# Performance work log

Measured on AMD Instinct MI355X. Metric: run time of the kernel, lower is better.

## Reference

```python
import jax, jax.numpy as jnp
import numpy as np

HEAD_SIZE = 64

def setup_inputs() -> dict:
    key = jax.random.key(0)
    k1, k2, k3, k4 = jax.random.split(key, 4)
    B, T, C, H = 8, 2048, 1024, HEAD_SIZE
    x = jax.random.normal(k1, (B, T, C), dtype=jnp.float32)
    attention_mask = jnp.ones((B, T), dtype=jnp.int32)
    # nn.Linear(C, H, bias=False): store as [C, H] so y = x @ W
    s = 1.0 / np.sqrt(C)
    Wk = jax.random.normal(k2, (C, H), dtype=jnp.float32) * s
    Wq = jax.random.normal(k3, (C, H), dtype=jnp.float32) * s
    Wv = jax.random.normal(k4, (C, H), dtype=jnp.float32) * s
    return {"x": x, "attention_mask": attention_mask, "Wk": Wk, "Wq": Wq, "Wv": Wv}

def reference(x, attention_mask, Wk, Wq, Wv):
    # x: [B, T, C]; projections -> [B, T, H]
    k = jnp.einsum('btc,ch->bth', x, Wk)
    q = jnp.einsum('btc,ch->bth', x, Wq)
    v = jnp.einsum('btc,ch->bth', x, Wv)
    scale = k.shape[-1] ** -0.5
    wei = jnp.einsum('bqh,bkh->bqk', q, k) * scale  # [B, T, T]
    mask = attention_mask[:, None, :]               # [B, 1, T] key-padding mask
    wei = jnp.where(mask == 0, -jnp.inf, wei)
    wei_soft = jax.nn.softmax(wei, axis=-1)
    # dropout p=0.0 (eval mode): identity
    out = jnp.einsum('bqk,bkh->bqh', wei_soft, v)   # [B, T, H]
    return out
```

## Files before the change

### kernel.cpp

```cpp
#include <hip/hip_runtime.h>
#include <hip/hip_bf16.h>

typedef __bf16 bf16;
typedef __bf16 bf16x4 __attribute__((ext_vector_type(4)));
typedef __bf16 bf16x8 __attribute__((ext_vector_type(8)));
typedef float f32x4 __attribute__((ext_vector_type(4)));

#define NB 8
#define NT 2048
#define NC 1024
#define NH 64

__device__ inline f32x4 zero4() {
    f32x4 z; z[0] = 0.f; z[1] = 0.f; z[2] = 0.f; z[3] = 0.f; return z;
}

__global__ __launch_bounds__(256) void pack_w(const float* __restrict__ Wq,
                                              const float* __restrict__ Wk,
                                              const float* __restrict__ Wv,
                                              bf16* __restrict__ Wt2) {
    const int g = blockIdx.x * 256 + threadIdx.x;
    const int l = g & 63;
    const int kc = (g >> 6) & 1;
    const int kt = (g >> 7) & 15;
    const int nf = g >> 11;
    const int n = nf * 16 + (l & 15);
    const int k0 = kt * 64 + kc * 32 + (l >> 4) * 8;
    const float* W = (n < 64) ? Wq : (n < 128) ? Wk : Wv;
    const int h = n & 63;
    bf16x8 o;
#pragma unroll
    for (int e = 0; e < 8; ++e) o[e] = (bf16)W[(k0 + e) * NH + h];
    *reinterpret_cast<bf16x8*>(Wt2 + (size_t)g * 8) = o;
}

__global__ __launch_bounds__(256, 2) void qkv_gemm(const float* __restrict__ x,
                                                   const bf16* __restrict__ Wt2,
                                                   bf16* __restrict__ qp,
                                                   bf16* __restrict__ kp2,
                                                   bf16* __restrict__ vt2) {
    __shared__ bf16 xs[2][64][72];
    const int tid = threadIdx.x;
    const int wave = tid >> 6, lane = tid & 63;
    const int l16 = lane & 15, lhi = lane >> 4;
    const int qh = wave & 1;
    const int ch = wave >> 1;
    const int row0 = blockIdx.x * 64;
    const bf16* wb = Wt2 + (size_t)ch * 98304 + lane * 8;

    f32x4 acc[2][6];
#pragma unroll
    for (int mr = 0; mr < 2; ++mr)
#pragma unroll
        for (int nf = 0; nf < 6; ++nf) acc[mr][nf] = zero4();

    const int sr = tid >> 4;
    const int sc = (tid & 15) * 4;

    float4 xv[3][4];
    bf16x8 bfr[2][12];

#define LOAD_X(SLOT, KT)  do { \
    _Pragma("unroll") for (int _i = 0; _i < 4; ++_i) \
        xv[SLOT][_i] = *reinterpret_cast<const float4*>( \
            &x[(size_t)(row0 + sr + _i * 16) * NC + (KT) * 64 + sc]); \
} while (0)

#define LOAD_B(SLOT, KT)  do { \
    _Pragma("unroll") for (int _nf = 0; _nf < 6; ++_nf) \
        _Pragma("unroll") for (int _kc = 0; _kc < 2; ++_kc) \
            bfr[SLOT][_nf * 2 + _kc] = *reinterpret_cast<const bf16x8*>( \
                wb + _nf * 16384 + (KT) * 1024 + _kc * 512); \
} while (0)

#define WRITE_XS(BUF, SLOT)  do { \
    _Pragma("unroll") for (int _i = 0; _i < 4; ++_i) { \
        bf16x4 _w; \
        _w[0] = (bf16)xv[SLOT][_i].x; _w[1] = (bf16)xv[SLOT][_i].y; \
        _w[2] = (bf16)xv[SLOT][_i].z; _w[3] = (bf16)xv[SLOT][_i].w; \
        *reinterpret_cast<bf16x4*>(&xs[BUF][sr + _i * 16][sc]) = _w; \
    } \
} while (0)

    LOAD_X(0, 0);
    LOAD_X(1, 1);
    LOAD_X(2, 2);
    LOAD_B(0, 0);
    WRITE_XS(0, 0);
    __syncthreads();

#pragma unroll
    for (int kt = 0; kt < 16; ++kt) {
        const int cur = kt & 1, nxt = cur ^ 1;
        if (kt < 13) LOAD_X(kt % 3, kt + 3);
        bf16x8 a[2][2];
#pragma unroll
        for (int mr = 0; mr < 2; ++mr)
#pragma unroll
            for (int kc = 0; kc < 2; ++kc)
                a[mr][kc] = *reinterpret_cast<const bf16x8*>(
                    &xs[cur][qh * 32 + mr * 16 + l16][kc * 32 + lhi * 8]);
        if (kt < 15) WRITE_XS(nxt, (kt + 1) % 3);
        if (kt < 15) LOAD_B(nxt, kt + 1);
        __syncthreads();
        __builtin_amdgcn_s_setprio(1);
#pragma unroll
        for (int nf = 0; nf < 6; ++nf)
#pragma unroll
            for (int kc = 0; kc < 2; ++kc)
#pragma unroll
                for (int mr = 0; mr < 2; ++mr)
                    acc[mr][nf] = __builtin_amdgcn_mfma_f32_16x16x32_bf16(
                        a[mr][kc], bfr[cur][nf * 2 + kc], acc[mr][nf], 0, 0, 0);
        __builtin_amdgcn_s_setprio(0);
    }
#undef LOAD_X
#undef LOAD_B
#undef WRITE_XS

#pragma unroll
    for (int mr = 0; mr < 2; ++mr)
#pragma unroll
    for (int nf = 0; nf < 6; ++nf) {
        const int col = ch * 96 + nf * 16 + l16;
#pragma unroll
        for (int r = 0; r < 4; ++r) {
            const int row = row0 + qh * 32 + mr * 16 + lhi * 4 + r;
            const bf16 val = (bf16)acc[mr][nf][r];
            const int bb = row >> 11, kv = row & (NT - 1);
            const int t = kv >> 6;
            if (col < 64) {
                qp[(size_t)row * NH + col] = val;
            } else if (col < 128) {
                const int h = col - 64;
                const int kvb = (kv >> 4) & 3;
                const int lK = ((h & 31) >> 3) * 16 + (kv & 15);
                kp2[((((size_t)(bb * 32 + t) * 4 + kvb) * 2 + (h >> 5)) * 64 + lK) * 8 + (h & 7)] = val;
            } else {
                const int h = col - 128;
                const int kcV = (kv >> 5) & 1;
                const int lV = ((kv & 31) >> 3) * 16 + (h & 15);
                vt2[((((size_t)(bb * 32 + t) * 2 + kcV) * 4 + (h >> 4)) * 64 + lV) * 8 + (kv & 7)] = val;
            }
        }
    }
}

__global__ __launch_bounds__(256, 2) void attn(const bf16* __restrict__ qp,
                                               const bf16* __restrict__ kp2,
                                               const bf16* __restrict__ vt2,
                                               const int* __restrict__ mask,
                                               float* __restrict__ out) {
    __shared__ __align__(16) char smem[4 * 2 * 16 * 68 * 4];
    bf16 (*p_lds)[64][20] = reinterpret_cast<bf16 (*)[64][20]>(smem);
    float (*sm_o)[2][16][68] = reinterpret_cast<float (*)[2][16][68]>(smem);
    __shared__ float sm_m[4][2][16], sm_l[4][2][16];

    const int tid = threadIdx.x;
    const int sp = tid >> 6, lane = tid & 63;
    const int l16 = lane & 15, lhi = lane >> 4;
    const int b = blockIdx.y;
    const int tb = sp * 8;
    bf16* const pw = &p_lds[sp][0][0];

    bf16x8 aq[2][2];
#pragma unroll
    for (int t = 0; t < 2; ++t)
#pragma unroll
        for (int hc = 0; hc < 2; ++hc)
            aq[t][hc] = *reinterpret_cast<const bf16x8*>(
                &qp[((size_t)b * NT + blockIdx.x * 32 + t * 16 + l16) * NH + hc * 32 + lhi * 8]);

    const bf16* kw = kp2 + (size_t)b * 131072 + (size_t)tb * 4096 + lane * 8;
    const bf16* vw = vt2 + (size_t)b * 131072 + (size_t)tb * 4096 + lane * 8;
    const int*  mw = mask + b * NT + tb * 64 + lhi * 4;

    float m[2] = {-1e30f, -1e30f}, l[2] = {0.f, 0.f};
    f32x4 o[2][4];
#pragma unroll
    for (int t = 0; t < 2; ++t)
#pragma unroll
        for (int hb = 0; hb < 4; ++hb) o[t][hb] = zero4();

#pragma unroll
    for (int it = 0; it < 8; ++it) {
        const int fo = it * 4096;
        bf16x8 kf[8];
#pragma unroll
        for (int i = 0; i < 8; ++i)
            kf[i] = *reinterpret_cast<const bf16x8*>(kw + fo + i * 512);
        int4 mv[4];
#pragma unroll
        for (int kvb = 0; kvb < 4; ++kvb)
            mv[kvb] = *reinterpret_cast<const int4*>(mw + it * 64 + kvb * 16);
        f32x4 s[2][4];
        __builtin_amdgcn_s_setprio(1);
#pragma unroll
        for (int t = 0; t < 2; ++t)
#pragma unroll
            for (int kvb = 0; kvb < 4; ++kvb) {
                s[t][kvb] = zero4();
                s[t][kvb] = __builtin_amdgcn_mfma_f32_16x16x32_bf16(kf[kvb * 2], aq[t][0], s[t][kvb], 0, 0, 0);
                s[t][kvb] = __builtin_amdgcn_mfma_f32_16x16x32_bf16(kf[kvb * 2 + 1], aq[t][1], s[t][kvb], 0, 0, 0);
            }
        __builtin_amdgcn_s_setprio(0);
        bf16x8 vf[8];
#pragma unroll
        for (int i = 0; i < 8; ++i)
            vf[i] = *reinterpret_cast<const bf16x8*>(vw + fo + i * 512);
#pragma unroll
        for (int t = 0; t < 2; ++t)
#pragma unroll
            for (int kvb = 0; kvb < 4; ++kvb) {
                s[t][kvb][0] = mv[kvb].x ? s[t][kvb][0] * 0.125f : -1e30f;
                s[t][kvb][1] = mv[kvb].y ? s[t][kvb][1] * 0.125f : -1e30f;
                s[t][kvb][2] = mv[kvb].z ? s[t][kvb][2] * 0.125f : -1e30f;
                s[t][kvb][3] = mv[kvb].w ? s[t][kvb][3] * 0.125f : -1e30f;
            }
#pragma unroll
        for (int t = 0; t < 2; ++t) {
            float tm = s[t][0][0];
#pragma unroll
            for (int kvb = 0; kvb < 4; ++kvb)
#pragma unroll
                for (int r = 0; r < 4; ++r) tm = fmaxf(tm, s[t][kvb][r]);
            tm = fmaxf(tm, __shfl_xor(tm, 16));
            tm = fmaxf(tm, __shfl_xor(tm, 32));
            const float mn = fmaxf(m[t], tm);
            const float alpha = __expf(m[t] - mn);
            m[t] = mn;
            float ps = 0.f;
#pragma unroll
            for (int kvb = 0; kvb < 4; ++kvb)
#pragma unroll
                for (int r = 0; r < 4; ++r) {
                    const float p = __expf(s[t][kvb][r] - m[t]);
                    s[t][kvb][r] = p;
                    ps += p;
                }
            ps += __shfl_xor(ps, 16);
            ps += __shfl_xor(ps, 32);
            l[t] = l[t] * alpha + ps;
#pragma unroll
            for (int kvb = 0; kvb < 4; ++kvb) {
                bf16x4 w;
                w[0] = (bf16)s[t][kvb][0]; w[1] = (bf16)s[t][kvb][1];
                w[2] = (bf16)s[t][kvb][2]; w[3] = (bf16)s[t][kvb][3];
                const int row = l16 + 16 * ((kvb * 2 + (lhi >> 1)) & 3);
                *reinterpret_cast<bf16x4*>(pw + row * 20 + (kvb >> 1) * 8 + (lhi & 1) * 4) = w;
            }
            float ar[4];
#pragma unroll
            for (int r = 0; r < 4; ++r) ar[r] = __shfl(alpha, lhi * 4 + r);
#pragma unroll
            for (int hb = 0; hb < 4; ++hb)
#pragma unroll
                for (int r = 0; r < 4; ++r) o[t][hb][r] *= ar[r];
            __builtin_amdgcn_s_setprio(1);
#pragma unroll
            for (int kc = 0; kc < 2; ++kc) {
                const bf16* pr = pw + lane * 20 + kc * 8;
                const bf16x4 lo = *reinterpret_cast<const bf16x4*>(pr);
                const bf16x4 hi = *reinterpret_cast<const bf16x4*>(pr + 4);
                const bf16x8 pa = __builtin_shufflevector(lo, hi, 0, 1, 2, 3, 4, 5, 6, 7);
#pragma unroll
                for (int hb = 0; hb < 4; ++hb)
                    o[t][hb] = __builtin_amdgcn_mfma_f32_16x16x32_bf16(pa, vf[kc * 4 + hb], o[t][hb], 0, 0, 0);
            }
            __builtin_amdgcn_s_setprio(0);
        }
    }

    __syncthreads();
#pragma unroll
    for (int t = 0; t < 2; ++t) {
#pragma unroll
        for (int hb = 0; hb < 4; ++hb)
#pragma unroll
            for (int r = 0; r < 4; ++r)
                sm_o[sp][t][lhi * 4 + r][hb * 16 + l16] = o[t][hb][r];
        if (lhi == 0) {
            sm_m[sp][t][l16] = m[t];
            sm_l[sp][t][l16] = l[t];
        }
    }
    __syncthreads();

#pragma unroll
    for (int e = 0; e < 8; ++e) {
        const int idx = e * 256 + tid;
        const int row = idx >> 6;
        const int col = idx & 63;
        const int t2 = row >> 4, r16 = row & 15;
        float M = sm_m[0][t2][r16];
#pragma unroll
        for (int s2 = 1; s2 < 4; ++s2) M = fmaxf(M, sm_m[s2][t2][r16]);
        float L = 0.f, accv = 0.f;
#pragma unroll
        for (int s2 = 0; s2 < 4; ++s2) {
            const float w = __expf(sm_m[s2][t2][r16] - M);
            L += w * sm_l[s2][t2][r16];
            accv += w * sm_o[s2][t2][r16][col];
        }
        out[((size_t)b * NT + blockIdx.x * 32 + row) * NH + col] = accv / L;
    }
}

extern "C" void kernel_launch(void* const* d_in, const int* in_sizes, int n_in,
                              void* d_out, int out_size, void* d_ws, size_t ws_size,
                              hipStream_t stream) {
    const float* x    = (const float*)d_in[0];
    const int*   mask = (const int*)d_in[1];
    const float* Wk   = (const float*)d_in[2];
    const float* Wq   = (const float*)d_in[3];
    const float* Wv   = (const float*)d_in[4];
    float* out = (float*)d_out;

    char* ws = (char*)d_ws;
    bf16* Wt2 = (bf16*)(ws);
    bf16* qp  = (bf16*)(ws + (512 << 10));
    bf16* kp2 = (bf16*)(ws + (512 << 10) + (2 << 20));
    bf16* vt2 = (bf16*)(ws + (512 << 10) + (4 << 20));

    pack_w<<<dim3(96), dim3(256), 0, stream>>>(Wq, Wk, Wv, Wt2);
    qkv_gemm<<<dim3(256), dim3(256), 0, stream>>>(x, Wt2, qp, kp2, vt2);
    attn<<<dim3(64, 8), dim3(256), 0, stream>>>(qp, kp2, vt2, mask, out);
}
```

Before: 48.10 us.

## Fold softmax scale into Wq, use exp2 with lazy rescale, widen QKV GEMM blocks

Wq is pre-multiplied by scale*log2(e) so attention can use exp2 without a per-score multiply. The mask becomes an additive bias, and the online-softmax rescale of the output and running sum is skipped unless the row max grows by more than 8 in log2 units. Separately, the QKV GEMM now uses 512 threads with each wave covering half the columns, lowering register pressure and raising wave count. The lazy rescale lets unnormalised values grow by up to 2^8 before correction, which adds some numerical risk. The 0.125 scale and the mask handling move out of the inner loop.

Measured after the change: 50.61 us. +5.2%, slower.

```diff
diff --git a/kernel.cpp b/kernel.cpp
--- a/kernel.cpp
+++ b/kernel.cpp
@@ -10,6 +10,8 @@
 #define NT 2048
 #define NC 1024
 #define NH 64
+
+#define QSCALE 0.18033688011112042f
 
 __device__ inline f32x4 zero4() {
     f32x4 z; z[0] = 0.f; z[1] = 0.f; z[2] = 0.f; z[3] = 0.f; return z;
@@ -27,14 +29,15 @@
     const int n = nf * 16 + (l & 15);
     const int k0 = kt * 64 + kc * 32 + (l >> 4) * 8;
     const float* W = (n < 64) ? Wq : (n < 128) ? Wk : Wv;
+    const float sc = (n < 64) ? QSCALE : 1.0f;
     const int h = n & 63;
     bf16x8 o;
 #pragma unroll
-    for (int e = 0; e < 8; ++e) o[e] = (bf16)W[(k0 + e) * NH + h];
+    for (int e = 0; e < 8; ++e) o[e] = (bf16)(W[(k0 + e) * NH + h] * sc);
     *reinterpret_cast<bf16x8*>(Wt2 + (size_t)g * 8) = o;
 }
 
-__global__ __launch_bounds__(256, 2) void qkv_gemm(const float* __restrict__ x,
+__global__ __launch_bounds__(512, 2) void qkv_gemm(const float* __restrict__ x,
                                                    const bf16* __restrict__ Wt2,
                                                    bf16* __restrict__ qp,
                                                    bf16* __restrict__ kp2,
@@ -46,40 +49,40 @@
     const int qh = wave & 1;
     const int ch = wave >> 1;
     const int row0 = blockIdx.x * 64;
-    const bf16* wb = Wt2 + (size_t)ch * 98304 + lane * 8;
-
-    f32x4 acc[2][6];
+    const bf16* wb = Wt2 + (size_t)(ch * 3) * 16384 + lane * 8;
+
+    f32x4 acc[2][3];
 #pragma unroll
     for (int mr = 0; mr < 2; ++mr)
 #pragma unroll
-        for (int nf = 0; nf < 6; ++nf) acc[mr][nf] = zero4();
+        for (int nf = 0; nf < 3; ++nf) acc[mr][nf] = zero4();
 
     const int sr = tid >> 4;
     const int sc = (tid & 15) * 4;
 
-    float4 xv[3][4];
-    bf16x8 bfr[2][12];
+    float4 xv[3][2];
+    bf16x8 bfr[2][6];
 
 #define LOAD_X(SLOT, KT)  do { \
-    _Pragma("unroll") for (int _i = 0; _i < 4; ++_i) \
-        xv[SLOT][_i] = *reinterpret_cast<const float4*>( \
-            &x[(size_t)(row0 + sr + _i * 16) * NC + (KT) * 64 + sc]); \
+    xv[SLOT][0] = *reinterpret_cast<const float4*>(&x[(size_t)(row0 + sr) * NC + (KT) * 64 + sc]); \
+    xv[SLOT][1] = *reinterpret_cast<const float4*>(&x[(size_t)(row0 + sr + 32) * NC + (KT) * 64 + sc]); \
 } while (0)
 
 #define LOAD_B(SLOT, KT)  do { \
-    _Pragma("unroll") for (int _nf = 0; _nf < 6; ++_nf) \
+    _Pragma("unroll") for (int _nf = 0; _nf < 3; ++_nf) \
         _Pragma("unroll") for (int _kc = 0; _kc < 2; ++_kc) \
             bfr[SLOT][_nf * 2 + _kc] = *reinterpret_cast<const bf16x8*>( \
                 wb + _nf * 16384 + (KT) * 1024 + _kc * 512); \
 } while (0)
 
 #define WRITE_XS(BUF, SLOT)  do { \
-    _Pragma("unroll") for (int _i = 0; _i < 4; ++_i) { \
-        bf16x4 _w; \
-        _w[0] = (bf16)xv[SLOT][_i].x; _w[1] = (bf16)xv[SLOT][_i].y; \
-        _w[2] = (bf16)xv[SLOT][_i].z; _w[3] = (bf16)xv[SLOT][_i].w; \
-        *reinterpret_cast<bf16x4*>(&xs[BUF][sr + _i * 16][sc]) = _w; \
-    } \
+    bf16x4 _w0, _w1; \
+    _w0[0] = (bf16)xv[SLOT][0].x; _w0[1] = (bf16)xv[SLOT][0].y; \
+    _w0[2] = (bf16)xv[SLOT][0].z; _w0[3] = (bf16)xv[SLOT][0].w; \
+    _w1[0] = (bf16)xv[SLOT][1].x; _w1[1] = (bf16)xv[SLOT][1].y; \
+    _w1[2] = (bf16)xv[SLOT][1].z; _w1[3] = (bf16)xv[SLOT][1].w; \
+    *reinterpret_cast<bf16x4*>(&xs[BUF][sr][sc]) = _w0; \
+    *reinterpret_cast<bf16x4*>(&xs[BUF][sr + 32][sc]) = _w1; \
 } while (0)
 
     LOAD_X(0, 0);
@@ -105,7 +108,7 @@
         __syncthreads();
         __builtin_amdgcn_s_setprio(1);
 #pragma unroll
-        for (int nf = 0; nf < 6; ++nf)
+        for (int nf = 0; nf < 3; ++nf)
 #pragma unroll
             for (int kc = 0; kc < 2; ++kc)
 #pragma unroll
@@ -121,8 +124,8 @@
 #pragma unroll
     for (int mr = 0; mr < 2; ++mr)
 #pragma unroll
-    for (int nf = 0; nf < 6; ++nf) {
-        const int col = ch * 96 + nf * 16 + l16;
+    for (int nf = 0; nf < 3; ++nf) {
+        const int col = ch * 48 + nf * 16 + l16;
 #pragma unroll
         for (int r = 0; r < 4; ++r) {
             const int row = row0 + qh * 32 + mr * 16 + lhi * 4 + r;
@@ -160,6 +163,7 @@
     const int sp = tid >> 6, lane = tid & 63;
     const int l16 = lane & 15, lhi = lane >> 4;
     const int b = blockIdx.y;
+    const int q_base = blockIdx.x * 32;
     const int tb = sp * 8;
     bf16* const pw = &p_lds[sp][0][0];
 
@@ -169,7 +173,7 @@
 #pragma unroll
         for (int hc = 0; hc < 2; ++hc)
             aq[t][hc] = *reinterpret_cast<const bf16x8*>(
-                &qp[((size_t)b * NT + blockIdx.x * 32 + t * 16 + l16) * NH + hc * 32 + lhi * 8]);
+                &qp[((size_t)b * NT + q_base + t * 16 + l16) * NH + hc * 32 + lhi * 8]);
 
     const bf16* kw = kp2 + (size_t)b * 131072 + (size_t)tb * 4096 + lane * 8;
     const bf16* vw = vt2 + (size_t)b * 131072 + (size_t)tb * 4096 + lane * 8;
@@ -208,17 +212,20 @@
 #pragma unroll
         for (int i = 0; i < 8; ++i)
             vf[i] = *reinterpret_cast<const bf16x8*>(vw + fo + i * 512);
-#pragma unroll
-        for (int t = 0; t < 2; ++t)
-#pragma unroll
-            for (int kvb = 0; kvb < 4; ++kvb) {
-                s[t][kvb][0] = mv[kvb].x ? s[t][kvb][0] * 0.125f : -1e30f;
-                s[t][kvb][1] = mv[kvb].y ? s[t][kvb][1] * 0.125f : -1e30f;
-                s[t][kvb][2] = mv[kvb].z ? s[t][kvb][2] * 0.125f : -1e30f;
-                s[t][kvb][3] = mv[kvb].w ? s[t][kvb][3] * 0.125f : -1e30f;
-            }
+        f32x4 bias;
+        bias[0] = mv[0].x ? 0.f : -1e30f;
+        f32x4 biasv[4];
+#pragma unroll
+        for (int kvb = 0; kvb < 4; ++kvb) {
+            biasv[kvb][0] = mv[kvb].x ? 0.f : -1e30f;
+            biasv[kvb][1] = mv[kvb].y ? 0.f : -1e30f;
+            biasv[kvb][2] = mv[kvb].z ? 0.f : -1e30f;
+            biasv[kvb][3] = mv[kvb].w ? 0.f : -1e30f;
+        }
 #pragma unroll
         for (int t = 0; t < 2; ++t) {
+#pragma unroll
+            for (int kvb = 0; kvb < 4; ++kvb) s[t][kvb] += biasv[kvb];
             float tm = s[t][0][0];
 #pragma unroll
             for (int kvb = 0; kvb < 4; ++kvb)
@@ -226,21 +233,31 @@
                 for (int r = 0; r < 4; ++r) tm = fmaxf(tm, s[t][kvb][r]);
             tm = fmaxf(tm, __shfl_xor(tm, 16));
             tm = fmaxf(tm, __shfl_xor(tm, 32));
-            const float mn = fmaxf(m[t], tm);
-            const float alpha = __expf(m[t] - mn);
-            m[t] = mn;
+            if (!__all(tm <= m[t] + 8.f)) {
+                const float mn = fmaxf(m[t], tm);
+                const float alpha = __builtin_exp2f(m[t] - mn);
+                m[t] = mn;
+                l[t] *= alpha;
+                float ar[4];
+#pragma unroll
+                for (int r = 0; r < 4; ++r) ar[r] = __shfl(alpha, lhi * 4 + r);
+#pragma unroll
+                for (int hb = 0; hb < 4; ++hb)
+#pragma unroll
+                    for (int r = 0; r < 4; ++r) o[t][hb][r] *= ar[r];
+            }
             float ps = 0.f;
 #pragma unroll
             for (int kvb = 0; kvb < 4; ++kvb)
 #pragma unroll
                 for (int r = 0; r < 4; ++r) {
-                    const float p = __expf(s[t][kvb][r] - m[t]);
+                    const float p = __builtin_exp2f(s[t][kvb][r] - m[t]);
                     s[t][kvb][r] = p;
                     ps += p;
                 }
             ps += __shfl_xor(ps, 16);
             ps += __shfl_xor(ps, 32);
-            l[t] = l[t] * alpha + ps;
+            l[t] += ps;
 #pragma unroll
             for (int kvb = 0; kvb < 4; ++kvb) {
                 bf16x4 w;
@@ -249,13 +266,6 @@
                 const int row = l16 + 16 * ((kvb * 2 + (lhi >> 1)) & 3);
                 *reinterpret_cast<bf16x4*>(pw + row * 20 + (kvb >> 1) * 8 + (lhi & 1) * 4) = w;
             }
-            float ar[4];
-#pragma unroll
-            for (int r = 0; r < 4; ++r) ar[r] = __shfl(alpha, lhi * 4 + r);
-#pragma unroll
-            for (int hb = 0; hb < 4; ++hb)
-#pragma unroll
-                for (int r = 0; r < 4; ++r) o[t][hb][r] *= ar[r];
             __builtin_amdgcn_s_setprio(1);
 #pragma unroll
             for (int kc = 0; kc < 2; ++kc) {
@@ -298,11 +308,11 @@
         float L = 0.f, accv = 0.f;
 #pragma unroll
         for (int s2 = 0; s2 < 4; ++s2) {
-            const float w = __expf(sm_m[s2][t2][r16] - M);
+            const float w = __builtin_exp2f(sm_m[s2][t2][r16] - M);
             L += w * sm_l[s2][t2][r16];
             accv += w * sm_o[s2][t2][r16][col];
         }
-        out[((size_t)b * NT + blockIdx.x * 32 + row) * NH + col] = accv / L;
+        out[((size_t)b * NT + q_base + row) * NH + col] = accv / L;
     }
 }
 
@@ -323,6 +333,6 @@
     bf16* vt2 = (bf16*)(ws + (512 << 10) + (4 << 20));
 
     pack_w<<<dim3(96), dim3(256), 0, stream>>>(Wq, Wk, Wv, Wt2);
-    qkv_gemm<<<dim3(256), dim3(256), 0, stream>>>(x, Wt2, qp, kp2, vt2);
+    qkv_gemm<<<dim3(256), dim3(512), 0, stream>>>(x, Wt2, qp, kp2, vt2);
     attn<<<dim3(64, 8), dim3(256), 0, stream>>>(qp, kp2, vt2, mask, out);
 }
```

## Fold softmax scale into Wq, lazy rescale, 8-wave split-KV attention

Applied to the files above, without the earlier changes.

Folds 1/sqrt(H)*log2(e) into the packed Wq weights so the attention kernel can use exp2 directly with no per-score multiply, and turns the mask into an additive bias. Adds a lazy online-softmax rescale that only updates the running max and rescales the accumulators when the new tile max exceeds the old one by more than 8. Doubles the attention block to 512 threads (8 waves, each covering 4 KV tiles instead of 8) and uses a 1D grid that interleaves batches. The cost is more LDS and a heavier cross-wave merge, plus bf16 rounding of the pre-scaled Q.

After: 55.70 us. 1.16x slower.

```diff
diff --git a/kernel.cpp b/kernel.cpp
--- a/kernel.cpp
+++ b/kernel.cpp
@@ -10,6 +10,8 @@
 #define NT 2048
 #define NC 1024
 #define NH 64
+
+#define QSCALE 0.18033688011112042f
 
 __device__ inline f32x4 zero4() {
     f32x4 z; z[0] = 0.f; z[1] = 0.f; z[2] = 0.f; z[3] = 0.f; return z;
@@ -27,10 +29,11 @@
     const int n = nf * 16 + (l & 15);
     const int k0 = kt * 64 + kc * 32 + (l >> 4) * 8;
     const float* W = (n < 64) ? Wq : (n < 128) ? Wk : Wv;
+    const float sc = (n < 64) ? QSCALE : 1.0f;
     const int h = n & 63;
     bf16x8 o;
 #pragma unroll
-    for (int e = 0; e < 8; ++e) o[e] = (bf16)W[(k0 + e) * NH + h];
+    for (int e = 0; e < 8; ++e) o[e] = (bf16)(W[(k0 + e) * NH + h] * sc);
     *reinterpret_cast<bf16x8*>(Wt2 + (size_t)g * 8) = o;
 }
 
@@ -146,21 +149,22 @@
     }
 }
 
-__global__ __launch_bounds__(256, 2) void attn(const bf16* __restrict__ qp,
+__global__ __launch_bounds__(512, 2) void attn(const bf16* __restrict__ qp,
                                                const bf16* __restrict__ kp2,
                                                const bf16* __restrict__ vt2,
                                                const int* __restrict__ mask,
                                                float* __restrict__ out) {
-    __shared__ __align__(16) char smem[4 * 2 * 16 * 68 * 4];
+    __shared__ __align__(16) char smem[8 * 2 * 16 * 68 * 4];
     bf16 (*p_lds)[64][20] = reinterpret_cast<bf16 (*)[64][20]>(smem);
     float (*sm_o)[2][16][68] = reinterpret_cast<float (*)[2][16][68]>(smem);
-    __shared__ float sm_m[4][2][16], sm_l[4][2][16];
+    __shared__ float sm_m[8][2][16], sm_l[8][2][16];
 
     const int tid = threadIdx.x;
     const int sp = tid >> 6, lane = tid & 63;
     const int l16 = lane & 15, lhi = lane >> 4;
-    const int b = blockIdx.y;
-    const int tb = sp * 8;
+    const int b = blockIdx.x & 7;
+    const int q_base = (blockIdx.x >> 3) * 32;
+    const int tb = sp * 4;
     bf16* const pw = &p_lds[sp][0][0];
 
     bf16x8 aq[2][2];
@@ -169,7 +173,7 @@
 #pragma unroll
         for (int hc = 0; hc < 2; ++hc)
             aq[t][hc] = *reinterpret_cast<const bf16x8*>(
-                &qp[((size_t)b * NT + blockIdx.x * 32 + t * 16 + l16) * NH + hc * 32 + lhi * 8]);
+                &qp[((size_t)b * NT + q_base + t * 16 + l16) * NH + hc * 32 + lhi * 8]);
 
     const bf16* kw = kp2 + (size_t)b * 131072 + (size_t)tb * 4096 + lane * 8;
     const bf16* vw = vt2 + (size_t)b * 131072 + (size_t)tb * 4096 + lane * 8;
@@ -183,7 +187,7 @@
         for (int hb = 0; hb < 4; ++hb) o[t][hb] = zero4();
 
 #pragma unroll
-    for (int it = 0; it < 8; ++it) {
+    for (int it = 0; it < 4; ++it) {
         const int fo = it * 4096;
         bf16x8 kf[8];
 #pragma unroll
@@ -208,17 +212,18 @@
 #pragma unroll
         for (int i = 0; i < 8; ++i)
             vf[i] = *reinterpret_cast<const bf16x8*>(vw + fo + i * 512);
-#pragma unroll
-        for (int t = 0; t < 2; ++t)
-#pragma unroll
-            for (int kvb = 0; kvb < 4; ++kvb) {
-                s[t][kvb][0] = mv[kvb].x ? s[t][kvb][0] * 0.125f : -1e30f;
-                s[t][kvb][1] = mv[kvb].y ? s[t][kvb][1] * 0.125f : -1e30f;
-                s[t][kvb][2] = mv[kvb].z ? s[t][kvb][2] * 0.125f : -1e30f;
-                s[t][kvb][3] = mv[kvb].w ? s[t][kvb][3] * 0.125f : -1e30f;
-            }
+        f32x4 biasv[4];
+#pragma unroll
+        for (int kvb = 0; kvb < 4; ++kvb) {
+            biasv[kvb][0] = mv[kvb].x ? 0.f : -1e30f;
+            biasv[kvb][1] = mv[kvb].y ? 0.f : -1e30f;
+            biasv[kvb][2] = mv[kvb].z ? 0.f : -1e30f;
+            biasv[kvb][3] = mv[kvb].w ? 0.f : -1e30f;
+        }
 #pragma unroll
         for (int t = 0; t < 2; ++t) {
+#pragma unroll
+            for (int kvb = 0; kvb < 4; ++kvb) s[t][kvb] += biasv[kvb];
             float tm = s[t][0][0];
 #pragma unroll
             for (int kvb = 0; kvb < 4; ++kvb)
@@ -226,21 +231,31 @@
                 for (int r = 0; r < 4; ++r) tm = fmaxf(tm, s[t][kvb][r]);
             tm = fmaxf(tm, __shfl_xor(tm, 16));
             tm = fmaxf(tm, __shfl_xor(tm, 32));
-            const float mn = fmaxf(m[t], tm);
-            const float alpha = __expf(m[t] - mn);
-            m[t] = mn;
+            if (!__all(tm <= m[t] + 8.f)) {
+                const float mn = fmaxf(m[t], tm);
+                const float alpha = __builtin_exp2f(m[t] - mn);
+                m[t] = mn;
+                l[t] *= alpha;
+                float ar[4];
+#pragma unroll
+                for (int r = 0; r < 4; ++r) ar[r] = __shfl(alpha, lhi * 4 + r);
+#pragma unroll
+                for (int hb = 0; hb < 4; ++hb)
+#pragma unroll
+                    for (int r = 0; r < 4; ++r) o[t][hb][r] *= ar[r];
+            }
             float ps = 0.f;
 #pragma unroll
             for (int kvb = 0; kvb < 4; ++kvb)
 #pragma unroll
                 for (int r = 0; r < 4; ++r) {
-                    const float p = __expf(s[t][kvb][r] - m[t]);
+                    const float p = __builtin_exp2f(s[t][kvb][r] - m[t]);
                     s[t][kvb][r] = p;
                     ps += p;
                 }
             ps += __shfl_xor(ps, 16);
             ps += __shfl_xor(ps, 32);
-            l[t] = l[t] * alpha + ps;
+            l[t] += ps;
 #pragma unroll
             for (int kvb = 0; kvb < 4; ++kvb) {
                 bf16x4 w;
@@ -249,13 +264,6 @@
                 const int row = l16 + 16 * ((kvb * 2 + (lhi >> 1)) & 3);
                 *reinterpret_cast<bf16x4*>(pw + row * 20 + (kvb >> 1) * 8 + (lhi & 1) * 4) = w;
             }
-            float ar[4];
-#pragma unroll
-            for (int r = 0; r < 4; ++r) ar[r] = __shfl(alpha, lhi * 4 + r);
-#pragma unroll
-            for (int hb = 0; hb < 4; ++hb)
-#pragma unroll
-                for (int r = 0; r < 4; ++r) o[t][hb][r] *= ar[r];
             __builtin_amdgcn_s_setprio(1);
 #pragma unroll
             for (int kc = 0; kc < 2; ++kc) {
@@ -287,22 +295,22 @@
     __syncthreads();
 
 #pragma unroll
-    for (int e = 0; e < 8; ++e) {
-        const int idx = e * 256 + tid;
+    for (int e = 0; e < 4; ++e) {
+        const int idx = e * 512 + tid;
         const int row = idx >> 6;
         const int col = idx & 63;
         const int t2 = row >> 4, r16 = row & 15;
         float M = sm_m[0][t2][r16];
 #pragma unroll
-        for (int s2 = 1; s2 < 4; ++s2) M = fmaxf(M, sm_m[s2][t2][r16]);
+        for (int s2 = 1; s2 < 8; ++s2) M = fmaxf(M, sm_m[s2][t2][r16]);
         float L = 0.f, accv = 0.f;
 #pragma unroll
-        for (int s2 = 0; s2 < 4; ++s2) {
-            const float w = __expf(sm_m[s2][t2][r16] - M);
+        for (int s2 = 0; s2 < 8; ++s2) {
+            const float w = __builtin_exp2f(sm_m[s2][t2][r16] - M);
             L += w * sm_l[s2][t2][r16];
             accv += w * sm_o[s2][t2][r16][col];
         }
-        out[((size_t)b * NT + blockIdx.x * 32 + row) * NH + col] = accv / L;
+        out[((size_t)b * NT + q_base + row) * NH + col] = accv / L;
     }
 }
 
@@ -324,5 +332,5 @@
 
     pack_w<<<dim3(96), dim3(256), 0, stream>>>(Wq, Wk, Wv, Wt2);
     qkv_gemm<<<dim3(256), dim3(256), 0, stream>>>(x, Wt2, qp, kp2, vt2);
-    attn<<<dim3(64, 8), dim3(256), 0, stream>>>(qp, kp2, vt2, mask, out);
-}
+    attn<<<dim3(512), dim3(512), 0, stream>>>(qp, kp2, vt2, mask, out);
+}
```
